# Optimization experiments

Hardware: AMD Instinct MI355X
Metric: run time of the kernel (lower is better)

The kernel has to match this reference:

```python
import jax, jax.numpy as jnp
import numpy as np

EPS = 1e-6   # param.eps
DT = 1e-2    # param.dt
DX = 1.0     # param.dx
DY = 1.0     # param.dy
N_PARAM = 1.0  # param.N


def _lap(c, dx=1.0, dy=1.0):
    # 5-point periodic Laplacian stencil on the last two dims
    return ((jnp.roll(c, 1, -1) + jnp.roll(c, -1, -1) - 2.0 * c) / (dx * dx)
            + (jnp.roll(c, 1, -2) + jnp.roll(c, -1, -2) - 2.0 * c) / (dy * dy))


def _log_with_mask(m, eps=EPS):
    # masked positions get constant eps -> zero gradient there, like torch masked_fill
    return jnp.log(jnp.where(m < eps, eps, m))


def setup_inputs() -> dict:
    key = jax.random.key(0)
    ks = jax.random.split(key, 12)
    B, H, W = 8, 1024, 1024
    inp = {
        "cv": jax.random.uniform(ks[0], (B, H, W), dtype=jnp.float32),
        "ci": jax.random.uniform(ks[1], (B, H, W), dtype=jnp.float32),
        "eta": jax.random.uniform(ks[2], (B, H, W), dtype=jnp.float32),
    }
    names = ["energy_v0", "energy_i0", "kBT0", "kappa_v0", "kappa_i0",
             "kappa_eta0", "diff_v0", "diff_i0", "L0"]
    for i, n in enumerate(names):
        inp[n] = jax.random.uniform(ks[3 + i], (1,), dtype=jnp.float32)
    return inp


def reference(cv, ci, eta, energy_v0, energy_i0, kBT0, kappa_v0, kappa_i0,
              kappa_eta0, diff_v0, diff_i0, L0):
    energy_v = jnp.abs(energy_v0) + 0.001
    energy_i = jnp.abs(energy_i0) + 0.001
    kBT = jnp.abs(kBT0) + 0.001
    kappa_v = jnp.abs(kappa_v0) + 0.001
    kappa_i = jnp.abs(kappa_i0) + 0.001
    kappa_eta = jnp.abs(kappa_eta0) + 0.001
    diff_v = jnp.abs(diff_v0) + 0.001
    diff_i = jnp.abs(diff_i0) + 0.001
    L = jnp.abs(L0) + 0.001

    lap_cv = _lap(cv, DX, DY)
    lap_ci = _lap(ci, DX, DY)
    lap_eta = _lap(eta, DX, DY)

    h = (eta - 1.0) ** 2
    j = eta ** 2
    cs = 1.0 - cv - ci
    log_cv = _log_with_mask(cv)
    log_ci = _log_with_mask(ci)
    log_cs = _log_with_mask(cs)

    fs = energy_v * cv + energy_i * ci + kBT * (cv * log_cv + ci * log_ci + cs * log_cs)
    dfs_dcv = energy_v + kBT * (log_cv - log_cs)
    dfs_dci = energy_i + kBT * (log_ci - log_cs)

    fv = (cv - 1.0) ** 2 + ci ** 2
    dfv_dcv = 2.0 * (cv - 1.0)
    dfv_dci = 2.0 * ci

    dF_dcv = h * dfs_dcv + j * dfv_dcv - kappa_v * lap_cv
    dF_dci = h * dfs_dci + j * dfv_dci - kappa_i * lap_ci
    dF_deta = N_PARAM * (fs * 2.0 * (eta - 1.0) + fv * 2.0 * eta - kappa_eta * lap_eta)

    mv = diff_v * cv / kBT
    mi = diff_i * ci / kBT

    cv_new = jnp.clip(cv + DT * (mv * _lap(dF_dcv)), 0.0, 1.0)
    ci_new = jnp.clip(ci + DT * (mi * _lap(dF_dci)), 0.0, 1.0)
    eta_new = jnp.clip(eta + DT * (-L * dF_deta), 0.0, 1.0)
    return cv_new, ci_new, eta_new
```

## Files before the change

### kernel.cpp

```cpp
#include <hip/hip_runtime.h>

#define WMASK 1023
#define LOG2W 10
#define HW (1024 * 1024)

#define EPS 1e-6f
#define DT 1e-2f

#define TX 64
#define TY 16
#define RX 72
#define RY 20
#define DXT 66
#define DYT 18

__device__ __forceinline__ float scal(const float* __restrict__ p) {
    return fabsf(p[0]) + 0.001f;
}
__device__ __forceinline__ float logm(float m) {
    return __logf(m < EPS ? EPS : m);
}
__device__ __forceinline__ float clip01(float v) {
    return fminf(fmaxf(v, 0.0f), 1.0f);
}

__global__ __launch_bounds__(256) void irr_fused(
    const float* __restrict__ cv,
    const float* __restrict__ ci,
    const float* __restrict__ eta,
    const float* __restrict__ p_ev,
    const float* __restrict__ p_ei,
    const float* __restrict__ p_kbt,
    const float* __restrict__ p_kv,
    const float* __restrict__ p_ki,
    const float* __restrict__ p_ke,
    const float* __restrict__ p_dv,
    const float* __restrict__ p_di,
    const float* __restrict__ p_L,
    float* __restrict__ cv_new,
    float* __restrict__ ci_new,
    float* __restrict__ eta_new)
{
    __shared__ float scv[RY][RX];
    __shared__ float sci[RY][RX];
    __shared__ float seta[RY][RX];
    __shared__ float sdv[DYT][DXT];
    __shared__ float sdi[DYT][DXT];

    const int tid = threadIdx.x;
    const int x0 = blockIdx.x * TX;
    const int y0 = blockIdx.y * TY;
    const int bbase = blockIdx.z * HW;

    const float energy_v = scal(p_ev);
    const float energy_i = scal(p_ei);
    const float kBT      = scal(p_kbt);
    const float kappa_v  = scal(p_kv);
    const float kappa_i  = scal(p_ki);
    const float kappa_e  = scal(p_ke);
    const float diff_v   = scal(p_dv);
    const float diff_i   = scal(p_di);
    const float L        = scal(p_L);
    const float rv = diff_v / kBT;
    const float ri = diff_i / kBT;

    for (int t = tid; t < 3 * 384; t += 256) {
        const int f = t / 384;
        const int r = t - f * 384;
        if (r < 360) {
            const int cx = r % 18;
            const int cy = r / 18;
            const int gx = (x0 - 4 + cx * 4) & WMASK;
            const int gy = (y0 - 2 + cy) & WMASK;
            const float* __restrict__ src = (f == 0) ? cv : (f == 1) ? ci : eta;
            const float4 v = *(const float4*)(src + bbase + (gy << LOG2W) + gx);
            float* dst = (f == 0) ? &scv[cy][cx * 4]
                       : (f == 1) ? &sci[cy][cx * 4]
                                  : &seta[cy][cx * 4];
            *(float4*)dst = v;
        }
    }
    __syncthreads();

    for (int t = tid; t < DXT * DYT; t += 256) {
        const int ex = t % DXT;
        const int ey = t / DXT;
        const int rx = ex + 3;
        const int ry = ey + 1;

        const float c0 = scv[ry][rx];
        const float lap_cv = scv[ry][rx - 1] + scv[ry][rx + 1]
                           + scv[ry - 1][rx] + scv[ry + 1][rx] - 4.0f * c0;
        const float i0 = sci[ry][rx];
        const float lap_ci = sci[ry][rx - 1] + sci[ry][rx + 1]
                           + sci[ry - 1][rx] + sci[ry + 1][rx] - 4.0f * i0;
        const float e0 = seta[ry][rx];
        const float lap_eta = seta[ry][rx - 1] + seta[ry][rx + 1]
                            + seta[ry - 1][rx] + seta[ry + 1][rx] - 4.0f * e0;

        const float h  = (e0 - 1.0f) * (e0 - 1.0f);
        const float jj = e0 * e0;
        const float cs = 1.0f - c0 - i0;
        const float lcv = logm(c0);
        const float lci = logm(i0);
        const float lcs = logm(cs);

        const float fs = energy_v * c0 + energy_i * i0
                       + kBT * (c0 * lcv + i0 * lci + cs * lcs);
        const float dfs_dcv = energy_v + kBT * (lcv - lcs);
        const float dfs_dci = energy_i + kBT * (lci - lcs);

        const float fv = (c0 - 1.0f) * (c0 - 1.0f) + i0 * i0;

        sdv[ey][ex] = h * dfs_dcv + jj * (2.0f * (c0 - 1.0f)) - kappa_v * lap_cv;
        sdi[ey][ex] = h * dfs_dci + jj * (2.0f * i0)          - kappa_i * lap_ci;

        if (ex >= 1 && ex <= TX && ey >= 1 && ey <= TY) {
            const float dF_deta = fs * 2.0f * (e0 - 1.0f) + fv * 2.0f * e0
                                - kappa_e * lap_eta;
            const int gidx = bbase + ((y0 + ey - 1) << LOG2W) + (x0 + ex - 1);
            __builtin_nontemporal_store(clip01(e0 + DT * (-L * dF_deta)),
                                        &eta_new[gidx]);
        }
    }
    __syncthreads();

    for (int t = tid; t < TX * TY; t += 256) {
        const int ox = t & (TX - 1);
        const int oy = t >> 6;
        const int ex = ox + 1;
        const int ey = oy + 1;

        const float v0 = sdv[ey][ex];
        const float lap_v = sdv[ey][ex - 1] + sdv[ey][ex + 1]
                          + sdv[ey - 1][ex] + sdv[ey + 1][ex] - 4.0f * v0;
        const float w0 = sdi[ey][ex];
        const float lap_i = sdi[ey][ex - 1] + sdi[ey][ex + 1]
                          + sdi[ey - 1][ex] + sdi[ey + 1][ex] - 4.0f * w0;

        const float c0 = scv[oy + 2][ox + 4];
        const float i0 = sci[oy + 2][ox + 4];

        const int gidx = bbase + ((y0 + oy) << LOG2W) + (x0 + ox);
        __builtin_nontemporal_store(clip01(c0 + DT * ((rv * c0) * lap_v)), &cv_new[gidx]);
        __builtin_nontemporal_store(clip01(i0 + DT * ((ri * i0) * lap_i)), &ci_new[gidx]);
    }
}

extern "C" void kernel_launch(void* const* d_in, const int* in_sizes, int n_in,
                              void* d_out, int out_size, void* d_ws, size_t ws_size,
                              hipStream_t stream) {
    const float* cv  = (const float*)d_in[0];
    const float* ci  = (const float*)d_in[1];
    const float* eta = (const float*)d_in[2];
    const float* p_ev  = (const float*)d_in[3];
    const float* p_ei  = (const float*)d_in[4];
    const float* p_kbt = (const float*)d_in[5];
    const float* p_kv  = (const float*)d_in[6];
    const float* p_ki  = (const float*)d_in[7];
    const float* p_ke  = (const float*)d_in[8];
    const float* p_dv  = (const float*)d_in[9];
    const float* p_di  = (const float*)d_in[10];
    const float* p_L   = (const float*)d_in[11];

    const int N = in_sizes[0];

    float* out     = (float*)d_out;
    float* cv_new  = out;
    float* ci_new  = out + N;
    float* eta_new = out + 2 * N;

    const dim3 block(256);
    const dim3 grid(1024 / TX, 1024 / TY, N / HW);

    irr_fused<<<grid, block, 0, stream>>>(cv, ci, eta, p_ev, p_ei, p_kbt,
                                          p_kv, p_ki, p_ke, p_dv, p_di, p_L,
                                          cv_new, ci_new, eta_new);
}
```

Before: 208.5 us.

## Compute first-stage stencil directly from global memory with float4 per-thread vectors

Removes the shared-memory staging of cv/ci/eta. Each thread now loads 4-wide vectors plus halo neighbours straight from global memory, computes the first-stage chemical potentials for four points, and writes them to shared memory as float4. The second stage is likewise vectorised to four outputs per thread with float4 stores, and one barrier is dropped. The cost is redundant global loads for up/down rows and scalar edge loads, which are expected to be served by cache.

```diff
diff --git a/kernel.cpp b/kernel.cpp
--- a/kernel.cpp
+++ b/kernel.cpp
@@ -9,10 +9,12 @@
 
 #define TX 64
 #define TY 16
-#define RX 72
-#define RY 20
-#define DXT 66
+
+#define DCH 18
 #define DYT 18
+#define DST 72
+
+typedef float f4 __attribute__((ext_vector_type(4)));
 
 __device__ __forceinline__ float scal(const float* __restrict__ p) {
     return fabsf(p[0]) + 0.001f;
@@ -41,11 +43,8 @@
     float* __restrict__ ci_new,
     float* __restrict__ eta_new)
 {
-    __shared__ float scv[RY][RX];
-    __shared__ float sci[RY][RX];
-    __shared__ float seta[RY][RX];
-    __shared__ float sdv[DYT][DXT];
-    __shared__ float sdi[DYT][DXT];
+    __shared__ float sdv[DYT][DST];
+    __shared__ float sdi[DYT][DST];
 
     const int tid = threadIdx.x;
     const int x0 = blockIdx.x * TX;
@@ -64,86 +63,123 @@
     const float rv = diff_v / kBT;
     const float ri = diff_i / kBT;
 
-    for (int t = tid; t < 3 * 384; t += 256) {
-        const int f = t / 384;
-        const int r = t - f * 384;
-        if (r < 360) {
-            const int cx = r % 18;
-            const int cy = r / 18;
-            const int gx = (x0 - 4 + cx * 4) & WMASK;
-            const int gy = (y0 - 2 + cy) & WMASK;
-            const float* __restrict__ src = (f == 0) ? cv : (f == 1) ? ci : eta;
-            const float4 v = *(const float4*)(src + bbase + (gy << LOG2W) + gx);
-            float* dst = (f == 0) ? &scv[cy][cx * 4]
-                       : (f == 1) ? &sci[cy][cx * 4]
-                                  : &seta[cy][cx * 4];
-            *(float4*)dst = v;
+    for (int t = tid; t < DCH * DYT; t += 256) {
+        const int ex4 = t % DCH;
+        const int ey  = t / DCH;
+        const int gx  = (x0 - 4 + (ex4 << 2)) & WMASK;
+        const int gxl = (gx - 1) & WMASK;
+        const int gxr = (gx + 4) & WMASK;
+        const int gy  = (y0 - 1 + ey) & WMASK;
+        const int rowC = bbase + (gy << LOG2W);
+        const int rowU = bbase + (((gy - 1) & WMASK) << LOG2W);
+        const int rowD = bbase + (((gy + 1) & WMASK) << LOG2W);
+
+        const f4    cC = *(const f4*)(cv + rowC + gx);
+        const float cL = cv[rowC + gxl];
+        const float cR = cv[rowC + gxr];
+        const f4    cU = *(const f4*)(cv + rowU + gx);
+        const f4    cD = *(const f4*)(cv + rowD + gx);
+
+        const f4    iC = *(const f4*)(ci + rowC + gx);
+        const float iL = ci[rowC + gxl];
+        const float iR = ci[rowC + gxr];
+        const f4    iU = *(const f4*)(ci + rowU + gx);
+        const f4    iD = *(const f4*)(ci + rowD + gx);
+
+        const f4    eC = *(const f4*)(eta + rowC + gx);
+        const float eL = eta[rowC + gxl];
+        const float eR = eta[rowC + gxr];
+        const f4    eU = *(const f4*)(eta + rowU + gx);
+        const f4    eD = *(const f4*)(eta + rowD + gx);
+
+        f4 dv, di, en;
+        #pragma unroll
+        for (int j = 0; j < 4; ++j) {
+            const float c0 = cC[j];
+            const float i0 = iC[j];
+            const float e0 = eC[j];
+            const float cl = (j == 0) ? cL : cC[j - 1];
+            const float cr = (j == 3) ? cR : cC[j + 1];
+            const float il = (j == 0) ? iL : iC[j - 1];
+            const float ir = (j == 3) ? iR : iC[j + 1];
+            const float el = (j == 0) ? eL : eC[j - 1];
+            const float er = (j == 3) ? eR : eC[j + 1];
+
+            const float lap_cv  = cl + cr + cU[j] + cD[j] - 4.0f * c0;
+            const float lap_ci  = il + ir + iU[j] + iD[j] - 4.0f * i0;
+            const float lap_eta = el + er + eU[j] + eD[j] - 4.0f * e0;
+
+            const float h  = (e0 - 1.0f) * (e0 - 1.0f);
+            const float jj = e0 * e0;
+            const float cs = 1.0f - c0 - i0;
+            const float lgv = logm(c0);
+            const float lgi = logm(i0);
+            const float lgs = logm(cs);
+
+            const float dfs_dcv = energy_v + kBT * (lgv - lgs);
+            const float dfs_dci = energy_i + kBT * (lgi - lgs);
+
+            dv[j] = h * dfs_dcv + jj * (2.0f * (c0 - 1.0f)) - kappa_v * lap_cv;
+            di[j] = h * dfs_dci + jj * (2.0f * i0)          - kappa_i * lap_ci;
+
+            const float fs = energy_v * c0 + energy_i * i0
+                           + kBT * (c0 * lgv + i0 * lgi + cs * lgs);
+            const float fv = (c0 - 1.0f) * (c0 - 1.0f) + i0 * i0;
+            const float dF_deta = fs * 2.0f * (e0 - 1.0f) + fv * 2.0f * e0
+                                - kappa_e * lap_eta;
+            en[j] = clip01(e0 + DT * (-L * dF_deta));
+        }
+
+        *(f4*)&sdv[ey][ex4 << 2] = dv;
+        *(f4*)&sdi[ey][ex4 << 2] = di;
+
+        if (ex4 >= 1 && ex4 <= 16 && ey >= 1 && ey <= 16) {
+            const int gidx = bbase + ((y0 - 1 + ey) << LOG2W)
+                           + (x0 - 4 + (ex4 << 2));
+            __builtin_nontemporal_store(en, (f4*)(eta_new + gidx));
         }
     }
     __syncthreads();
 
-    for (int t = tid; t < DXT * DYT; t += 256) {
-        const int ex = t % DXT;
-        const int ey = t / DXT;
-        const int rx = ex + 3;
-        const int ry = ey + 1;
-
-        const float c0 = scv[ry][rx];
-        const float lap_cv = scv[ry][rx - 1] + scv[ry][rx + 1]
-                           + scv[ry - 1][rx] + scv[ry + 1][rx] - 4.0f * c0;
-        const float i0 = sci[ry][rx];
-        const float lap_ci = sci[ry][rx - 1] + sci[ry][rx + 1]
-                           + sci[ry - 1][rx] + sci[ry + 1][rx] - 4.0f * i0;
-        const float e0 = seta[ry][rx];
-        const float lap_eta = seta[ry][rx - 1] + seta[ry][rx + 1]
-                            + seta[ry - 1][rx] + seta[ry + 1][rx] - 4.0f * e0;
-
-        const float h  = (e0 - 1.0f) * (e0 - 1.0f);
-        const float jj = e0 * e0;
-        const float cs = 1.0f - c0 - i0;
-        const float lcv = logm(c0);
-        const float lci = logm(i0);
-        const float lcs = logm(cs);
-
-        const float fs = energy_v * c0 + energy_i * i0
-                       + kBT * (c0 * lcv + i0 * lci + cs * lcs);
-        const float dfs_dcv = energy_v + kBT * (lcv - lcs);
-        const float dfs_dci = energy_i + kBT * (lci - lcs);
-
-        const float fv = (c0 - 1.0f) * (c0 - 1.0f) + i0 * i0;
-
-        sdv[ey][ex] = h * dfs_dcv + jj * (2.0f * (c0 - 1.0f)) - kappa_v * lap_cv;
-        sdi[ey][ex] = h * dfs_dci + jj * (2.0f * i0)          - kappa_i * lap_ci;
-
-        if (ex >= 1 && ex <= TX && ey >= 1 && ey <= TY) {
-            const float dF_deta = fs * 2.0f * (e0 - 1.0f) + fv * 2.0f * e0
-                                - kappa_e * lap_eta;
-            const int gidx = bbase + ((y0 + ey - 1) << LOG2W) + (x0 + ex - 1);
-            __builtin_nontemporal_store(clip01(e0 + DT * (-L * dF_deta)),
-                                        &eta_new[gidx]);
+    {
+        const int ox4 = tid & 15;
+        const int oy  = tid >> 4;
+        const int ex  = (ox4 << 2) + 4;
+        const int ey  = oy + 1;
+
+        const f4    vC = *(const f4*)&sdv[ey][ex];
+        const float vL = sdv[ey][ex - 1];
+        const float vR = sdv[ey][ex + 4];
+        const f4    vU = *(const f4*)&sdv[ey - 1][ex];
+        const f4    vD = *(const f4*)&sdv[ey + 1][ex];
+
+        const f4    wC = *(const f4*)&sdi[ey][ex];
+        const float wL = sdi[ey][ex - 1];
+        const float wR = sdi[ey][ex + 4];
+        const f4    wU = *(const f4*)&sdi[ey - 1][ex];
+        const f4    wD = *(const f4*)&sdi[ey + 1][ex];
+
+        const int gx = x0 + (ox4 << 2);
+        const int gy = y0 + oy;
+        const int gidx = bbase + (gy << LOG2W) + gx;
+
+        const f4 c0 = *(const f4*)(cv + gidx);
+        const f4 i0 = *(const f4*)(ci + gidx);
+
+        f4 outv, outi;
+        #pragma unroll
+        for (int j = 0; j < 4; ++j) {
+            const float lv = ((j == 0) ? vL : vC[j - 1])
+                           + ((j == 3) ? vR : vC[j + 1])
+                           + vU[j] + vD[j] - 4.0f * vC[j];
+            const float li = ((j == 0) ? wL : wC[j - 1])
+                           + ((j == 3) ? wR : wC[j + 1])
+                           + wU[j] + wD[j] - 4.0f * wC[j];
+            outv[j] = clip01(c0[j] + DT * ((rv * c0[j]) * lv));
+            outi[j] = clip01(i0[j] + DT * ((ri * i0[j]) * li));
         }
-    }
-    __syncthreads();
-
-    for (int t = tid; t < TX * TY; t += 256) {
-        const int ox = t & (TX - 1);
-        const int oy = t >> 6;
-        const int ex = ox + 1;
-        const int ey = oy + 1;
-
-        const float v0 = sdv[ey][ex];
-        const float lap_v = sdv[ey][ex - 1] + sdv[ey][ex + 1]
-                          + sdv[ey - 1][ex] + sdv[ey + 1][ex] - 4.0f * v0;
-        const float w0 = sdi[ey][ex];
-        const float lap_i = sdi[ey][ex - 1] + sdi[ey][ex + 1]
-                          + sdi[ey - 1][ex] + sdi[ey + 1][ex] - 4.0f * w0;
-
-        const float c0 = scv[oy + 2][ox + 4];
-        const float i0 = sci[oy + 2][ox + 4];
-
-        const int gidx = bbase + ((y0 + oy) << LOG2W) + (x0 + ox);
-        __builtin_nontemporal_store(clip01(c0 + DT * ((rv * c0) * lap_v)), &cv_new[gidx]);
-        __builtin_nontemporal_store(clip01(i0 + DT * ((ri * i0) * lap_i)), &ci_new[gidx]);
+        __builtin_nontemporal_store(outv, (f4*)(cv_new + gidx));
+        __builtin_nontemporal_store(outi, (f4*)(ci_new + gidx));
     }
 }
 
```

New measurement: 223.8 us. +7.3%, slower.
